# Kernel tuning notes

Measured on AMD Instinct MI355X. Metric: run time of the kernel, lower is better.

## Reference

```python
import jax, jax.numpy as jnp
import numpy as np

H, DQK, DV, DM, POS = 8, 64, 64, 768, 64

def _rel_basis(l, n):
    # Enformer central-mask relative position basis: [l, l, n]
    pos = jnp.arange(l)
    distance = pos[None, :] - pos[:, None]              # [l, l] int
    half = n // 2
    pow_rate = jnp.exp(jnp.log(jnp.asarray((l + 1) / 2.0, jnp.float32)) / half)
    center_widths = pow_rate ** jnp.arange(1, half + 1, dtype=jnp.float32)  # [half]
    unsigned = (jnp.abs(distance)[:, :, None].astype(jnp.float32) <= center_widths)
    signed = jnp.sign(distance)[:, :, None] * unsigned
    return jnp.concatenate([unsigned.astype(jnp.float32), signed.astype(jnp.float32)], axis=-1)

def setup_inputs() -> dict:
    key = jax.random.key(0)
    ks = jax.random.split(key, 9)
    b, l = 2, 1024
    x = jax.random.normal(ks[0], (b, l, DM), jnp.float32)
    # torch Linear weights: [out, in]
    Wq = jax.random.normal(ks[1], (H * DQK, DM), jnp.float32) * (1.0 / np.sqrt(DM))
    Wk = jax.random.normal(ks[2], (H * DQK, DM), jnp.float32) * (1.0 / np.sqrt(DM))
    Wv = jax.random.normal(ks[3], (H * DV, DM), jnp.float32) * (1.0 / np.sqrt(DM))
    Wo = jax.random.normal(ks[4], (DM, H * DV), jnp.float32) * (1.0 / np.sqrt(H * DV))
    bo = jnp.zeros((DM,), jnp.float32)
    u_bias = jax.random.normal(ks[5], (H, DQK), jnp.float32) * np.sqrt(2.0 / DQK)
    v_bias = jax.random.normal(ks[6], (H, DQK), jnp.float32) * np.sqrt(2.0 / DQK)
    w_pos = jax.random.normal(ks[7], (H, DQK, POS), jnp.float32) * np.sqrt(2.0 / POS)
    return {"x": x, "Wq": Wq, "Wk": Wk, "Wv": Wv, "Wo": Wo, "bo": bo,
            "u_bias": u_bias, "v_bias": v_bias, "w_pos": w_pos}

def reference(x, Wq, Wk, Wv, Wo, bo, u_bias, v_bias, w_pos):
    b, l, _ = x.shape
    q = (x @ Wq.T).reshape(b, l, H, DQK)
    k = (x @ Wk.T).reshape(b, l, H, DQK)
    v = (x @ Wv.T).reshape(b, l, H, DV)
    basis = _rel_basis(l, POS)                           # [l, l, n]
    scale = 1.0 / np.sqrt(DQK)
    # qr_term: einsum('bihd,hdn,ijn->bhij') factored to avoid [b,h,l,l,d]
    qw = jnp.einsum('bihd,hdn->bhin', q, w_pos)          # [b,h,l,n]
    qr = jnp.einsum('bhin,ijn->bhij', qw, basis)
    uk = jnp.einsum('hd,bjhd->bhj', u_bias, k)[:, :, None, :]
    vw = jnp.einsum('hd,hdn->hn', v_bias, w_pos)
    vr = jnp.einsum('hn,ijn->hij', vw, basis)[None]      # [1,h,l,l]
    bias = (qr + uk + vr) * scale
    scores = jnp.einsum('bihd,bjhd->bhij', q, k) * scale + bias
    attn = jax.nn.softmax(scores, axis=-1)
    out = jnp.einsum('bhij,bjhd->bihd', attn, v).reshape(b, l, H * DV)
    return out @ Wo.T + bo
```

## Files before the change

### kernel.cpp

```cpp
#include <hip/hip_runtime.h>

#define LSEQ 1024
#define NB   2
#define NH   8
#define DD   64
#define DMOD 768

using bf16x8 = __attribute__((ext_vector_type(8))) short;
using f32x4  = __attribute__((ext_vector_type(4))) float;

__device__ inline unsigned short f2bf(float f) {
    union { float f; unsigned u; } v; v.f = f;
    unsigned r = v.u + 0x7FFFu + ((v.u >> 16) & 1u);
    return (unsigned short)(r >> 16);
}

__global__ __launch_bounds__(256) void pack_setup(
    const float4* __restrict__ x,  const float4* __restrict__ wq,
    const float4* __restrict__ wk, const float4* __restrict__ wv,
    const float4* __restrict__ wo,
    const float* __restrict__ u_bias, const float* __restrict__ v_bias,
    const float* __restrict__ w_pos,
    ushort4* __restrict__ xb, ushort4* __restrict__ wqb, ushort4* __restrict__ wkb,
    ushort4* __restrict__ wvb, ushort4* __restrict__ wob,
    float* __restrict__ wsfx, unsigned char* __restrict__ cls_g)
{
    int tid = threadIdx.x;
    if (blockIdx.x >= 3072) {
        int sb = blockIdx.x - 3072;
        if (sb == 0) {
            __shared__ float w_s[32];
            __shared__ int cmin_s[1024];
            if (tid < 32) {
                float pr = expf(logf(512.5f) / 32.0f);
                w_s[tid] = powf(pr, (float)(tid + 1));
            }
            __syncthreads();
            for (int d = tid; d < 1024; d += 256) {
                float fd = (float)d;
                int cm = 32;
                for (int c = 31; c >= 0; --c) if (fd <= w_s[c]) cm = c;
                cmin_s[d] = cm;
            }
            __syncthreads();
            for (int d2 = tid; d2 < 2048; d2 += 256) {
                int dd = d2 - 1023;
                int ad = dd < 0 ? -dd : dd; if (ad > 1023) ad = 1023;
                int t = (dd < 0) ? 0 : ((dd == 0) ? 1 : 2);
                cls_g[d2] = (unsigned char)(t * 33 + cmin_s[ad]);
            }
        } else {
            int h = sb - 1;
            __shared__ float vred[4][64];
            __shared__ float ured[4][64];
            __shared__ float wd[64];
            int n = tid & 63, g = tid >> 6;
            float vs = 0.f, us = 0.f;
#pragma unroll
            for (int k = 0; k < 16; ++k) {
                int d = g * 16 + k;
                float wp = w_pos[(h * 64 + d) * 64 + n];
                vs += v_bias[h * 64 + d] * wp;
                us += u_bias[h * 64 + d] * wp;
            }
            vred[g][n] = vs; ured[g][n] = us;
            __syncthreads();
            if (tid < 64) {
                float v4 = vred[0][tid] + vred[1][tid] + vred[2][tid] + vred[3][tid];
                float u4 = ured[0][tid] + ured[1][tid] + ured[2][tid] + ured[3][tid];
                wd[tid] = v4 - u4;
            }
            __syncthreads();
            if (tid < 64) {
                int nn = tid & 31, cb = tid & 32;
                float s = 0.f;
                for (int c = 31; c >= nn; --c) s += wd[cb + c];
                wsfx[h * 64 + tid] = s * 0.125f;
            }
        }
        return;
    }
    int i = blockIdx.x * 256 + tid;
    const float4* src; ushort4* dst; int off;
    if (i < 393216)      { src = x;  dst = xb;  off = i; }
    else if (i < 491520) { src = wq; dst = wqb; off = i - 393216; }
    else if (i < 589824) { src = wk; dst = wkb; off = i - 491520; }
    else if (i < 688128) { src = wv; dst = wvb; off = i - 589824; }
    else                 { src = wo; dst = wob; off = i - 688128; }
    float4 v = src[off];
    ushort4 o;
    o.x = f2bf(v.x); o.y = f2bf(v.y); o.z = f2bf(v.z); o.w = f2bf(v.w);
    dst[off] = o;
}

__global__ __launch_bounds__(256) void gemm_qkv(
    const unsigned short* __restrict__ X, const unsigned short* __restrict__ W,
    const float* __restrict__ ub,
    unsigned short* __restrict__ Qb, unsigned short* __restrict__ Kb,
    unsigned short* __restrict__ Vtb)
{
    __shared__ __align__(16) unsigned short Xs[2][64][72];
    __shared__ __align__(16) unsigned short Wsm[2][64][72];
    __shared__ __align__(16) unsigned short Ct[64][72];

    int tid = threadIdx.x;
    int w = tid >> 6, lane = tid & 63, l15 = lane & 15, q = lane >> 4;
    int M0 = blockIdx.y * 64, N0 = blockIdx.x * 64;
    int rs = tid >> 3, seg = tid & 3 ? (tid & 7) : (tid & 7);
    seg = tid & 7;

    const unsigned short* xp = X + (size_t)(M0 + rs) * 768 + seg * 8;
    const unsigned short* wp = W + (size_t)(N0 + rs) * 768 + seg * 8;

    uint4 xa = *(const uint4*)(xp);
    uint4 xb = *(const uint4*)(xp + (size_t)32 * 768);
    uint4 wa = *(const uint4*)(wp);
    uint4 wb = *(const uint4*)(wp + (size_t)32 * 768);

    f32x4 acc[4] = {};
    int cur = 0;
    for (int k0 = 0; k0 < 768; k0 += 64) {
        *(uint4*)&Xs[cur][rs][seg * 8]       = xa;
        *(uint4*)&Xs[cur][rs + 32][seg * 8]  = xb;
        *(uint4*)&Wsm[cur][rs][seg * 8]      = wa;
        *(uint4*)&Wsm[cur][rs + 32][seg * 8] = wb;
        __syncthreads();
        if (k0 + 64 < 768) {
            xa = *(const uint4*)(xp + k0 + 64);
            xb = *(const uint4*)(xp + (size_t)32 * 768 + k0 + 64);
            wa = *(const uint4*)(wp + k0 + 64);
            wb = *(const uint4*)(wp + (size_t)32 * 768 + k0 + 64);
        }
        bf16x8 a0 = *(bf16x8*)&Xs[cur][w * 16 + l15][q * 8];
        bf16x8 a1 = *(bf16x8*)&Xs[cur][w * 16 + l15][32 + q * 8];
#pragma unroll
        for (int ct = 0; ct < 4; ++ct) {
            bf16x8 b0 = *(bf16x8*)&Wsm[cur][ct * 16 + l15][q * 8];
            bf16x8 b1 = *(bf16x8*)&Wsm[cur][ct * 16 + l15][32 + q * 8];
            acc[ct] = __builtin_amdgcn_mfma_f32_16x16x32_bf16(a0, b0, acc[ct], 0, 0, 0);
            acc[ct] = __builtin_amdgcn_mfma_f32_16x16x32_bf16(a1, b1, acc[ct], 0, 0, 0);
        }
        cur ^= 1;
    }

    if (N0 < 1024) {
        int isQ = (N0 < 512);
#pragma unroll
        for (int ct = 0; ct < 4; ++ct) {
            float u0 = isQ ? ub[N0 + ct * 16 + l15] : 0.f;
            float sc = isQ ? 0.125f : 1.0f;
#pragma unroll
            for (int r = 0; r < 4; ++r)
                Ct[w * 16 + q * 4 + r][ct * 16 + l15] = f2bf((acc[ct][r] + u0) * sc);
        }
        __syncthreads();
        int Nh = isQ ? N0 : (N0 - 512);
        unsigned short* out = isQ ? Qb : Kb;
        size_t base = ((size_t)((M0 >> 10) * 8 + (Nh >> 6)) * 1024 + (M0 & 1023)) * 64;
#pragma unroll
        for (int it = 0; it < 2; ++it) {
            int idx = tid + it * 256;
            int row = idx >> 3, sg = idx & 7;
            *(uint4*)(out + base + (size_t)row * 64 + sg * 8) = *(uint4*)&Ct[row][sg * 8];
        }
    } else {
#pragma unroll
        for (int ct = 0; ct < 4; ++ct) {
            ushort4 pk;
            pk.x = f2bf(acc[ct][0]); pk.y = f2bf(acc[ct][1]);
            pk.z = f2bf(acc[ct][2]); pk.w = f2bf(acc[ct][3]);
            *(ushort4*)&Ct[ct * 16 + l15][w * 16 + q * 4] = pk;
        }
        __syncthreads();
        size_t base = ((size_t)((M0 >> 10) * 8 + ((N0 - 1024) >> 6))) * 65536;
        int j0 = M0 & 1023;
#pragma unroll
        for (int it = 0; it < 2; ++it) {
            int idx = tid + it * 256;
            int d = idx >> 3, sg = idx & 7;
            *(uint4*)(Vtb + base + (size_t)d * 1024 + j0 + sg * 8) = *(uint4*)&Ct[d][sg * 8];
        }
    }
}

__global__ __launch_bounds__(256) void gemm_o(
    const unsigned short* __restrict__ X, const unsigned short* __restrict__ W,
    const float* __restrict__ bias, float* __restrict__ out)
{
    __shared__ __align__(16) unsigned short Xs[2][64][72];
    __shared__ __align__(16) unsigned short Wsm[2][64][72];
    __shared__ __align__(16) float Ctf[64][72];

    int tid = threadIdx.x;
    int w = tid >> 6, lane = tid & 63, l15 = lane & 15, q = lane >> 4;
    int M0 = blockIdx.y * 64, N0 = blockIdx.x * 64;
    int rs = tid >> 3, seg = tid & 7;

    const unsigned short* xp = X + (size_t)(M0 + rs) * 512 + seg * 8;
    const unsigned short* wp = W + (size_t)(N0 + rs) * 512 + seg * 8;

    uint4 xa = *(const uint4*)(xp);
    uint4 xb = *(const uint4*)(xp + (size_t)32 * 512);
    uint4 wa = *(const uint4*)(wp);
    uint4 wb = *(const uint4*)(wp + (size_t)32 * 512);

    f32x4 acc[4] = {};
    int cur = 0;
    for (int k0 = 0; k0 < 512; k0 += 64) {
        *(uint4*)&Xs[cur][rs][seg * 8]       = xa;
        *(uint4*)&Xs[cur][rs + 32][seg * 8]  = xb;
        *(uint4*)&Wsm[cur][rs][seg * 8]      = wa;
        *(uint4*)&Wsm[cur][rs + 32][seg * 8] = wb;
        __syncthreads();
        if (k0 + 64 < 512) {
            xa = *(const uint4*)(xp + k0 + 64);
            xb = *(const uint4*)(xp + (size_t)32 * 512 + k0 + 64);
            wa = *(const uint4*)(wp + k0 + 64);
            wb = *(const uint4*)(wp + (size_t)32 * 512 + k0 + 64);
        }
        bf16x8 a0 = *(bf16x8*)&Xs[cur][w * 16 + l15][q * 8];
        bf16x8 a1 = *(bf16x8*)&Xs[cur][w * 16 + l15][32 + q * 8];
#pragma unroll
        for (int ct = 0; ct < 4; ++ct) {
            bf16x8 b0 = *(bf16x8*)&Wsm[cur][ct * 16 + l15][q * 8];
            bf16x8 b1 = *(bf16x8*)&Wsm[cur][ct * 16 + l15][32 + q * 8];
            acc[ct] = __builtin_amdgcn_mfma_f32_16x16x32_bf16(a0, b0, acc[ct], 0, 0, 0);
            acc[ct] = __builtin_amdgcn_mfma_f32_16x16x32_bf16(a1, b1, acc[ct], 0, 0, 0);
        }
        cur ^= 1;
    }
#pragma unroll
    for (int ct = 0; ct < 4; ++ct) {
        float bv = bias[N0 + ct * 16 + l15];
#pragma unroll
        for (int r = 0; r < 4; ++r)
            Ctf[w * 16 + q * 4 + r][ct * 16 + l15] = acc[ct][r] + bv;
    }
    __syncthreads();
#pragma unroll
    for (int it = 0; it < 4; ++it) {
        int idx = tid + it * 256;
        int row = idx >> 4, sg = idx & 15;
        *(float4*)(out + (size_t)(M0 + row) * 768 + N0 + sg * 4) = *(float4*)&Ctf[row][sg * 4];
    }
}

__global__ __launch_bounds__(256, 4) void attn_mfma(
    const unsigned short* __restrict__ Qbf,
    const unsigned short* __restrict__ Kbf,
    const unsigned short* __restrict__ Vt,
    const float* __restrict__ w_pos,
    const float* __restrict__ wsfx,
    const unsigned char* __restrict__ cls_g,
    unsigned short* __restrict__ ao)
{
    __shared__ float biasT[16 * 99];
    __shared__ unsigned char cls[2048];
    __shared__ unsigned short Pl[4][16][76];
    union Ovl {
        struct { unsigned short wptS[64][68]; float qwL[16][68]; } pre;
        struct { float Obuf[4][64][17]; float lbuf[4][16]; } post;
    };
    __shared__ Ovl ovl;

    int tid = threadIdx.x;
    int b = blockIdx.z, h = blockIdx.y, bh = b * 8 + h;
    int i0 = blockIdx.x * 16;
    int w = tid >> 6, lane = tid & 63, l15 = lane & 15, q = lane >> 4;

    for (int idx = tid; idx < 512; idx += 256)
        ((unsigned int*)cls)[idx] = ((const unsigned int*)cls_g)[idx];
    {
        const float4* wsrc = (const float4*)(w_pos + h * 4096);
#pragma unroll
        for (int it = 0; it < 4; ++it) {
            int f = tid + it * 256;
            float4 wv = wsrc[f];
            int d = f >> 4, n4 = (f & 15) * 4;
            ovl.pre.wptS[n4 + 0][d] = f2bf(wv.x);
            ovl.pre.wptS[n4 + 1][d] = f2bf(wv.y);
            ovl.pre.wptS[n4 + 2][d] = f2bf(wv.z);
            ovl.pre.wptS[n4 + 3][d] = f2bf(wv.w);
        }
    }

    int ig = i0 + l15;
    const unsigned short* qrow = Qbf + ((size_t)bh * 1024 + ig) * 64;
    bf16x8 qf0 = *(const bf16x8*)(qrow + q * 8);
    bf16x8 qf1 = *(const bf16x8*)(qrow + 32 + q * 8);
    __syncthreads();

    {
        bf16x8 b0 = *(bf16x8*)&ovl.pre.wptS[w * 16 + l15][q * 8];
        bf16x8 b1 = *(bf16x8*)&ovl.pre.wptS[w * 16 + l15][32 + q * 8];
        f32x4 a = {};
        a = __builtin_amdgcn_mfma_f32_16x16x32_bf16(qf0, b0, a, 0, 0, 0);
        a = __builtin_amdgcn_mfma_f32_16x16x32_bf16(qf1, b1, a, 0, 0, 0);
#pragma unroll
        for (int r = 0; r < 4; ++r)
            ovl.pre.qwL[q * 4 + r][w * 16 + l15] = a[r];
    }
    __syncthreads();

    const float* wsh = wsfx + h * 64;
#pragma unroll
    for (int it = 0; it < 4; ++it) {
        int idx = tid + it * 256;
        int il = idx >> 6, n = idx & 63, nn = n & 31, cb = n & 32;
        float run = 0.f, s = 0.f;
#pragma unroll
        for (int c = 31; c >= 0; --c) {
            run += ovl.pre.qwL[il][cb + c];
            if (c == nn) s = run;
        }
        ovl.pre.qwL[il][n] = s + wsh[n];
    }
    __syncthreads();

    for (int idx = tid; idx < 528; idx += 256) {
        int il = idx / 33, c = idx - il * 33;
        float up = 0.f, sp = 0.f;
        if (c < 32) {
            up = ovl.pre.qwL[il][c];
            sp = ovl.pre.qwL[il][32 + c];
        }
        float* bt = biasT + il * 99;
        bt[c]      = up - sp;
        bt[33 + c] = up;
        bt[66 + c] = up + sp;
    }
    __syncthreads();

    const unsigned short* Kbase = Kbf + (size_t)bh * 65536;
    const unsigned short* Vbase = Vt  + (size_t)bh * 65536;
    const float* btrow = biasT + l15 * 99;
    int clsoff = 1023 - ig;

    f32x4 Oacc[4] = {};
    float lsum = 0.f;

    for (int jt = 0; jt < 4; ++jt) {
        int jb = w * 256 + jt * 64;
        f32x4 st[4];
        __builtin_amdgcn_s_setprio(1);
#pragma unroll
        for (int ct = 0; ct < 4; ++ct) {
            const unsigned short* krow = Kbase + (size_t)(jb + ct * 16 + l15) * 64;
            bf16x8 ka0 = *(const bf16x8*)(krow + q * 8);
            bf16x8 ka1 = *(const bf16x8*)(krow + 32 + q * 8);
            f32x4 a = {};
            a = __builtin_amdgcn_mfma_f32_16x16x32_bf16(ka0, qf0, a, 0, 0, 0);
            a = __builtin_amdgcn_mfma_f32_16x16x32_bf16(ka1, qf1, a, 0, 0, 0);
            st[ct] = a;
        }
        __builtin_amdgcn_s_setprio(0);
#pragma unroll
        for (int ct = 0; ct < 4; ++ct) {
            int d2b = jb + ct * 16 + q * 4 + clsoff;
            float pv[4];
#pragma unroll
            for (int r = 0; r < 4; ++r) {
                float s = st[ct][r] + btrow[cls[d2b + r]];
                float p = __expf(s);
                lsum += p;
                pv[r] = p;
            }
            ushort4 pk;
            pk.x = f2bf(pv[0]); pk.y = f2bf(pv[1]);
            pk.z = f2bf(pv[2]); pk.w = f2bf(pv[3]);
            *(ushort4*)&Pl[w][l15][ct * 16 + q * 4] = pk;
        }
        __builtin_amdgcn_s_setprio(1);
#pragma unroll
        for (int ks = 0; ks < 2; ++ks) {
            bf16x8 pb = *(const bf16x8*)&Pl[w][l15][ks * 32 + q * 8];
#pragma unroll
            for (int dt = 0; dt < 4; ++dt) {
                bf16x8 va = *(const bf16x8*)(Vbase + (size_t)(dt * 16 + l15) * 1024
                                             + jb + ks * 32 + q * 8);
                Oacc[dt] = __builtin_amdgcn_mfma_f32_16x16x32_bf16(va, pb, Oacc[dt], 0, 0, 0);
            }
        }
        __builtin_amdgcn_s_setprio(0);
    }

    lsum += __shfl_xor(lsum, 16);
    lsum += __shfl_xor(lsum, 32);

    __syncthreads();
#pragma unroll
    for (int dt = 0; dt < 4; ++dt)
#pragma unroll
        for (int r = 0; r < 4; ++r)
            ovl.post.Obuf[w][dt * 16 + q * 4 + r][l15] = Oacc[dt][r];
    if (lane < 16) ovl.post.lbuf[w][l15] = lsum;
    __syncthreads();

    for (int t2 = tid; t2 < 1024; t2 += 256) {
        int il = t2 >> 6, d = t2 & 63;
        float o = ovl.post.Obuf[0][d][il] + ovl.post.Obuf[1][d][il]
                + ovl.post.Obuf[2][d][il] + ovl.post.Obuf[3][d][il];
        float l = ovl.post.lbuf[0][il] + ovl.post.lbuf[1][il]
                + ovl.post.lbuf[2][il] + ovl.post.lbuf[3][il];
        ao[((size_t)(b * 1024 + i0 + il)) * 512 + h * 64 + d] = f2bf(o / l);
    }
}

extern "C" void kernel_launch(void* const* d_in, const int* in_sizes, int n_in,
                              void* d_out, int out_size, void* d_ws, size_t ws_size,
                              hipStream_t stream)
{
    const float* x      = (const float*)d_in[0];
    const float* Wq     = (const float*)d_in[1];
    const float* Wk     = (const float*)d_in[2];
    const float* Wv     = (const float*)d_in[3];
    const float* Wo     = (const float*)d_in[4];
    const float* bo     = (const float*)d_in[5];
    const float* u_bias = (const float*)d_in[6];
    const float* v_bias = (const float*)d_in[7];
    const float* w_pos  = (const float*)d_in[8];
    float* out = (float*)d_out;

    char* ws = (char*)d_ws;
    unsigned short* Xbf  = (unsigned short*)ws;            ws += 3145728;
    unsigned short* Wqkv = (unsigned short*)ws;            ws += 2359296;
    unsigned short* Wob  = (unsigned short*)ws;            ws += 786432;
    unsigned short* Qbf  = (unsigned short*)ws;            ws += 2097152;
    unsigned short* Kbf  = (unsigned short*)ws;            ws += 2097152;
    unsigned short* Vtb  = (unsigned short*)ws;            ws += 2097152;
    unsigned short* aob  = (unsigned short*)ws;            ws += 2097152;
    float*          wsfx = (float*)ws;                     ws += 2048;
    unsigned char*  clsg = (unsigned char*)ws;             ws += 2048;

    pack_setup<<<3081, 256, 0, stream>>>(
        (const float4*)x, (const float4*)Wq, (const float4*)Wk,
        (const float4*)Wv, (const float4*)Wo,
        u_bias, v_bias, w_pos,
        (ushort4*)Xbf,
        (ushort4*)Wqkv, (ushort4*)Wqkv + 98304, (ushort4*)Wqkv + 196608,
        (ushort4*)Wob,
        wsfx, clsg);

    gemm_qkv<<<dim3(24, 32), 256, 0, stream>>>(Xbf, Wqkv, u_bias, Qbf, Kbf, Vtb);

    attn_mfma<<<dim3(64, 8, 2), 256, 0, stream>>>(
        Qbf, Kbf, Vtb, w_pos, wsfx, clsg, aob);

    gemm_o<<<dim3(12, 32), 256, 0, stream>>>(aob, Wob, bo, out);
}
```

Baseline: 133.1 us.

## Split qw/bias-table prologue out of attention into a separate kernel

Moves the per-row q·w_pos projection, suffix-sum and bias-table construction from the attention kernel's prologue into a new qw_bias kernel that writes a per-row 99-entry bias table to global workspace. The attention kernel then only copies its 16 rows of that table into shared memory, dropping three barriers and the shared union. The suffix sum now uses warp shuffles instead of a serial 32-step loop. In exchange this adds a kernel launch and about 6.5 MB of extra global writes and reads.

Result: slower. 140.1 us (+5.3%).

```diff
diff --git a/kernel.cpp b/kernel.cpp
--- a/kernel.cpp
+++ b/kernel.cpp
@@ -106,8 +106,7 @@
     int tid = threadIdx.x;
     int w = tid >> 6, lane = tid & 63, l15 = lane & 15, q = lane >> 4;
     int M0 = blockIdx.y * 64, N0 = blockIdx.x * 64;
-    int rs = tid >> 3, seg = tid & 3 ? (tid & 7) : (tid & 7);
-    seg = tid & 7;
+    int rs = tid >> 3, seg = tid & 7;
 
     const unsigned short* xp = X + (size_t)(M0 + rs) * 768 + seg * 8;
     const unsigned short* wp = W + (size_t)(N0 + rs) * 768 + seg * 8;
@@ -245,23 +244,86 @@
     }
 }
 
+__global__ __launch_bounds__(256) void qw_bias(
+    const unsigned short* __restrict__ Qbf,
+    const float* __restrict__ w_pos,
+    const float* __restrict__ wsfx,
+    float* __restrict__ bias_g)
+{
+    __shared__ unsigned short wptS[64][68];
+    __shared__ float qwL[64][68];
+
+    int tid = threadIdx.x;
+    int bh = blockIdx.y, h = bh & 7;
+    int i0 = blockIdx.x * 64;
+    int w = tid >> 6, lane = tid & 63, l15 = lane & 15, q = lane >> 4;
+
+    const float4* wsrc = (const float4*)(w_pos + h * 4096);
+#pragma unroll
+    for (int it = 0; it < 4; ++it) {
+        int f = tid + it * 256;
+        float4 wv4 = wsrc[f];
+        int d = f >> 4, n4 = (f & 15) * 4;
+        wptS[n4 + 0][d] = f2bf(wv4.x);
+        wptS[n4 + 1][d] = f2bf(wv4.y);
+        wptS[n4 + 2][d] = f2bf(wv4.z);
+        wptS[n4 + 3][d] = f2bf(wv4.w);
+    }
+    int ig = i0 + w * 16 + l15;
+    const unsigned short* qrow = Qbf + ((size_t)bh * 1024 + ig) * 64;
+    bf16x8 qf0 = *(const bf16x8*)(qrow + q * 8);
+    bf16x8 qf1 = *(const bf16x8*)(qrow + 32 + q * 8);
+    __syncthreads();
+
+#pragma unroll
+    for (int ct = 0; ct < 4; ++ct) {
+        bf16x8 b0 = *(bf16x8*)&wptS[ct * 16 + l15][q * 8];
+        bf16x8 b1 = *(bf16x8*)&wptS[ct * 16 + l15][32 + q * 8];
+        f32x4 a = {};
+        a = __builtin_amdgcn_mfma_f32_16x16x32_bf16(qf0, b0, a, 0, 0, 0);
+        a = __builtin_amdgcn_mfma_f32_16x16x32_bf16(qf1, b1, a, 0, 0, 0);
+#pragma unroll
+        for (int r = 0; r < 4; ++r)
+            qwL[w * 16 + q * 4 + r][ct * 16 + l15] = a[r];
+    }
+    __syncthreads();
+
+    float wv = wsfx[h * 64 + lane];
+    int c = lane & 31;
+    for (int rr = 0; rr < 16; ++rr) {
+        int i = w * 16 + rr;
+        float s = qwL[i][lane];
+#pragma unroll
+        for (int off = 1; off < 32; off <<= 1) {
+            float t = __shfl_down(s, off, 32);
+            if (c + off < 32) s += t;
+        }
+        s += wv;
+        float o = __shfl_xor(s, 32);
+        float* bt = bias_g + ((size_t)bh * 1024 + i0 + i) * 99;
+        if (lane < 32) {
+            bt[c]      = s - o;
+            bt[33 + c] = s;
+            bt[66 + c] = s + o;
+        } else if (lane == 32) {
+            bt[32] = 0.f; bt[65] = 0.f; bt[98] = 0.f;
+        }
+    }
+}
+
 __global__ __launch_bounds__(256, 4) void attn_mfma(
     const unsigned short* __restrict__ Qbf,
     const unsigned short* __restrict__ Kbf,
     const unsigned short* __restrict__ Vt,
-    const float* __restrict__ w_pos,
-    const float* __restrict__ wsfx,
+    const float* __restrict__ bias_g,
     const unsigned char* __restrict__ cls_g,
     unsigned short* __restrict__ ao)
 {
     __shared__ float biasT[16 * 99];
     __shared__ unsigned char cls[2048];
     __shared__ unsigned short Pl[4][16][76];
-    union Ovl {
-        struct { unsigned short wptS[64][68]; float qwL[16][68]; } pre;
-        struct { float Obuf[4][64][17]; float lbuf[4][16]; } post;
-    };
-    __shared__ Ovl ovl;
+    __shared__ float Obuf[4][64][17];
+    __shared__ float lbuf[4][16];
 
     int tid = threadIdx.x;
     int b = blockIdx.z, h = blockIdx.y, bh = b * 8 + h;
@@ -271,64 +333,15 @@
     for (int idx = tid; idx < 512; idx += 256)
         ((unsigned int*)cls)[idx] = ((const unsigned int*)cls_g)[idx];
     {
-        const float4* wsrc = (const float4*)(w_pos + h * 4096);
-#pragma unroll
-        for (int it = 0; it < 4; ++it) {
-            int f = tid + it * 256;
-            float4 wv = wsrc[f];
-            int d = f >> 4, n4 = (f & 15) * 4;
-            ovl.pre.wptS[n4 + 0][d] = f2bf(wv.x);
-            ovl.pre.wptS[n4 + 1][d] = f2bf(wv.y);
-            ovl.pre.wptS[n4 + 2][d] = f2bf(wv.z);
-            ovl.pre.wptS[n4 + 3][d] = f2bf(wv.w);
-        }
+        const float* src = bias_g + ((size_t)bh * 1024 + i0) * 99;
+        for (int idx = tid; idx < 1584; idx += 256)
+            biasT[idx] = src[idx];
     }
 
     int ig = i0 + l15;
     const unsigned short* qrow = Qbf + ((size_t)bh * 1024 + ig) * 64;
     bf16x8 qf0 = *(const bf16x8*)(qrow + q * 8);
     bf16x8 qf1 = *(const bf16x8*)(qrow + 32 + q * 8);
-    __syncthreads();
-
-    {
-        bf16x8 b0 = *(bf16x8*)&ovl.pre.wptS[w * 16 + l15][q * 8];
-        bf16x8 b1 = *(bf16x8*)&ovl.pre.wptS[w * 16 + l15][32 + q * 8];
-        f32x4 a = {};
-        a = __builtin_amdgcn_mfma_f32_16x16x32_bf16(qf0, b0, a, 0, 0, 0);
-        a = __builtin_amdgcn_mfma_f32_16x16x32_bf16(qf1, b1, a, 0, 0, 0);
-#pragma unroll
-        for (int r = 0; r < 4; ++r)
-            ovl.pre.qwL[q * 4 + r][w * 16 + l15] = a[r];
-    }
-    __syncthreads();
-
-    const float* wsh = wsfx + h * 64;
-#pragma unroll
-    for (int it = 0; it < 4; ++it) {
-        int idx = tid + it * 256;
-        int il = idx >> 6, n = idx & 63, nn = n & 31, cb = n & 32;
-        float run = 0.f, s = 0.f;
-#pragma unroll
-        for (int c = 31; c >= 0; --c) {
-            run += ovl.pre.qwL[il][cb + c];
-            if (c == nn) s = run;
-        }
-        ovl.pre.qwL[il][n] = s + wsh[n];
-    }
-    __syncthreads();
-
-    for (int idx = tid; idx < 528; idx += 256) {
-        int il = idx / 33, c = idx - il * 33;
-        float up = 0.f, sp = 0.f;
-        if (c < 32) {
-            up = ovl.pre.qwL[il][c];
-            sp = ovl.pre.qwL[il][32 + c];
-        }
-        float* bt = biasT + il * 99;
-        bt[c]      = up - sp;
-        bt[33 + c] = up;
-        bt[66 + c] = up + sp;
-    }
     __syncthreads();
 
     const unsigned short* Kbase = Kbf + (size_t)bh * 65536;
@@ -387,21 +400,20 @@
     lsum += __shfl_xor(lsum, 16);
     lsum += __shfl_xor(lsum, 32);
 
-    __syncthreads();
 #pragma unroll
     for (int dt = 0; dt < 4; ++dt)
 #pragma unroll
         for (int r = 0; r < 4; ++r)
-            ovl.post.Obuf[w][dt * 16 + q * 4 + r][l15] = Oacc[dt][r];
-    if (lane < 16) ovl.post.lbuf[w][l15] = lsum;
+            Obuf[w][dt * 16 + q * 4 + r][l15] = Oacc[dt][r];
+    if (lane < 16) lbuf[w][l15] = lsum;
     __syncthreads();
 
     for (int t2 = tid; t2 < 1024; t2 += 256) {
         int il = t2 >> 6, d = t2 & 63;
-        float o = ovl.post.Obuf[0][d][il] + ovl.post.Obuf[1][d][il]
-                + ovl.post.Obuf[2][d][il] + ovl.post.Obuf[3][d][il];
-        float l = ovl.post.lbuf[0][il] + ovl.post.lbuf[1][il]
-                + ovl.post.lbuf[2][il] + ovl.post.lbuf[3][il];
+        float o = Obuf[0][d][il] + Obuf[1][d][il]
+                + Obuf[2][d][il] + Obuf[3][d][il];
+        float l = lbuf[0][il] + lbuf[1][il]
+                + lbuf[2][il] + lbuf[3][il];
         ao[((size_t)(b * 1024 + i0 + il)) * 512 + h * 64 + d] = f2bf(o / l);
     }
 }
@@ -431,6 +443,7 @@
     unsigned short* aob  = (unsigned short*)ws;            ws += 2097152;
     float*          wsfx = (float*)ws;                     ws += 2048;
     unsigned char*  clsg = (unsigned char*)ws;             ws += 2048;
+    float*          biasg = (float*)ws;                    ws += 6488064;
 
     pack_setup<<<3081, 256, 0, stream>>>(
         (const float4*)x, (const float4*)Wq, (const float4*)Wk,
@@ -443,8 +456,10 @@
 
     gemm_qkv<<<dim3(24, 32), 256, 0, stream>>>(Xbf, Wqkv, u_bias, Qbf, Kbf, Vtb);
 
+    qw_bias<<<dim3(16, 16), 256, 0, stream>>>(Qbf, w_pos, wsfx, biasg);
+
     attn_mfma<<<dim3(64, 8, 2), 256, 0, stream>>>(
-        Qbf, Kbf, Vtb, w_pos, wsfx, clsg, aob);
+        Qbf, Kbf, Vtb, biasg, clsg, aob);
 
     gemm_o<<<dim3(12, 32), 256, 0, stream>>>(aob, Wob, bo, out);
 }
```

## Fuse fp32-to-bf16 packing into QKV and output GEMM loaders, drop pack kernel

Applied to the files above, without the earlier changes.

Removes the separate pack_setup kernel. The GEMMs now read fp32 x and the weights directly and convert them to bf16 while staging tiles into shared memory. The small setup work (the position-class table and the per-head bias suffix sums) moves into an extra row of blocks in the QKV GEMM grid, reusing its shared memory. This saves one kernel launch and the round trip of writing and re-reading bf16 copies, but each GEMM block now loads twice as many bytes per tile, and the weights are converted again by every M-tile.

After: 134.3 us. About the same (+0.9%).

```diff
diff --git a/kernel.cpp b/kernel.cpp
--- a/kernel.cpp
+++ b/kernel.cpp
@@ -15,22 +15,37 @@
     return (unsigned short)(r >> 16);
 }
 
-__global__ __launch_bounds__(256) void pack_setup(
-    const float4* __restrict__ x,  const float4* __restrict__ wq,
-    const float4* __restrict__ wk, const float4* __restrict__ wv,
-    const float4* __restrict__ wo,
-    const float* __restrict__ u_bias, const float* __restrict__ v_bias,
+__device__ inline uint4 pk8(float4 a, float4 b) {
+    uint4 o;
+    o.x = (unsigned)f2bf(a.x) | ((unsigned)f2bf(a.y) << 16);
+    o.y = (unsigned)f2bf(a.z) | ((unsigned)f2bf(a.w) << 16);
+    o.z = (unsigned)f2bf(b.x) | ((unsigned)f2bf(b.y) << 16);
+    o.w = (unsigned)f2bf(b.z) | ((unsigned)f2bf(b.w) << 16);
+    return o;
+}
+
+__global__ __launch_bounds__(256) void gemm_qkv(
+    const float* __restrict__ X,
+    const float* __restrict__ Wqp, const float* __restrict__ Wkp,
+    const float* __restrict__ Wvp,
+    const float* __restrict__ ub,
+    const float* __restrict__ v_bias,
     const float* __restrict__ w_pos,
-    ushort4* __restrict__ xb, ushort4* __restrict__ wqb, ushort4* __restrict__ wkb,
-    ushort4* __restrict__ wvb, ushort4* __restrict__ wob,
+    unsigned short* __restrict__ Qb, unsigned short* __restrict__ Kb,
+    unsigned short* __restrict__ Vtb,
     float* __restrict__ wsfx, unsigned char* __restrict__ cls_g)
 {
+    __shared__ __align__(16) unsigned short Xs[2][64][72];
+    __shared__ __align__(16) unsigned short Wsm[2][64][72];
+    __shared__ __align__(16) unsigned short Ct[64][72];
+
     int tid = threadIdx.x;
-    if (blockIdx.x >= 3072) {
-        int sb = blockIdx.x - 3072;
+
+    if (blockIdx.y == 32) {
+        int sb = blockIdx.x;
         if (sb == 0) {
-            __shared__ float w_s[32];
-            __shared__ int cmin_s[1024];
+            float* w_s   = (float*)&Ct[0][0];
+            int*   cmin_s = (int*)&Ct[1][0];
             if (tid < 32) {
                 float pr = expf(logf(512.5f) / 32.0f);
                 w_s[tid] = powf(pr, (float)(tid + 1));
@@ -49,11 +64,11 @@
                 int t = (dd < 0) ? 0 : ((dd == 0) ? 1 : 2);
                 cls_g[d2] = (unsigned char)(t * 33 + cmin_s[ad]);
             }
-        } else {
+        } else if (sb <= 8) {
             int h = sb - 1;
-            __shared__ float vred[4][64];
-            __shared__ float ured[4][64];
-            __shared__ float wd[64];
+            float (*vred)[64] = (float(*)[64])&Ct[0][0];
+            float (*ured)[64] = (float(*)[64])&Ct[8][0];
+            float* wd = (float*)&Ct[16][0];
             int n = tid & 63, g = tid >> 6;
             float vs = 0.f, us = 0.f;
 #pragma unroll
@@ -61,7 +76,7 @@
                 int d = g * 16 + k;
                 float wp = w_pos[(h * 64 + d) * 64 + n];
                 vs += v_bias[h * 64 + d] * wp;
-                us += u_bias[h * 64 + d] * wp;
+                us += ub[h * 64 + d] * wp;
             }
             vred[g][n] = vs; ured[g][n] = us;
             __syncthreads();
@@ -80,57 +95,38 @@
         }
         return;
     }
-    int i = blockIdx.x * 256 + tid;
-    const float4* src; ushort4* dst; int off;
-    if (i < 393216)      { src = x;  dst = xb;  off = i; }
-    else if (i < 491520) { src = wq; dst = wqb; off = i - 393216; }
-    else if (i < 589824) { src = wk; dst = wkb; off = i - 491520; }
-    else if (i < 688128) { src = wv; dst = wvb; off = i - 589824; }
-    else                 { src = wo; dst = wob; off = i - 688128; }
-    float4 v = src[off];
-    ushort4 o;
-    o.x = f2bf(v.x); o.y = f2bf(v.y); o.z = f2bf(v.z); o.w = f2bf(v.w);
-    dst[off] = o;
-}
-
-__global__ __launch_bounds__(256) void gemm_qkv(
-    const unsigned short* __restrict__ X, const unsigned short* __restrict__ W,
-    const float* __restrict__ ub,
-    unsigned short* __restrict__ Qb, unsigned short* __restrict__ Kb,
-    unsigned short* __restrict__ Vtb)
-{
-    __shared__ __align__(16) unsigned short Xs[2][64][72];
-    __shared__ __align__(16) unsigned short Wsm[2][64][72];
-    __shared__ __align__(16) unsigned short Ct[64][72];
-
-    int tid = threadIdx.x;
+
     int w = tid >> 6, lane = tid & 63, l15 = lane & 15, q = lane >> 4;
     int M0 = blockIdx.y * 64, N0 = blockIdx.x * 64;
-    int rs = tid >> 3, seg = tid & 3 ? (tid & 7) : (tid & 7);
-    seg = tid & 7;
-
-    const unsigned short* xp = X + (size_t)(M0 + rs) * 768 + seg * 8;
-    const unsigned short* wp = W + (size_t)(N0 + rs) * 768 + seg * 8;
-
-    uint4 xa = *(const uint4*)(xp);
-    uint4 xb = *(const uint4*)(xp + (size_t)32 * 768);
-    uint4 wa = *(const uint4*)(wp);
-    uint4 wb = *(const uint4*)(wp + (size_t)32 * 768);
+    int rs = tid >> 3, seg = tid & 7;
+
+    const float* Wsrc; int Nr;
+    if (N0 < 512)       { Wsrc = Wqp; Nr = N0; }
+    else if (N0 < 1024) { Wsrc = Wkp; Nr = N0 - 512; }
+    else                { Wsrc = Wvp; Nr = N0 - 1024; }
+
+    const float* xp = X    + (size_t)(M0 + rs) * 768 + seg * 8;
+    const float* wp = Wsrc + (size_t)(Nr + rs) * 768 + seg * 8;
+
+    float4 xa0, xa1, xb0, xb1, wa0, wa1, wb0, wb1;
+#define LOADQ(K) do { \
+    xa0 = *(const float4*)(xp + (K));               xa1 = *(const float4*)(xp + (K) + 4); \
+    xb0 = *(const float4*)(xp + 32 * 768 + (K));    xb1 = *(const float4*)(xp + 32 * 768 + (K) + 4); \
+    wa0 = *(const float4*)(wp + (K));               wa1 = *(const float4*)(wp + (K) + 4); \
+    wb0 = *(const float4*)(wp + 32 * 768 + (K));    wb1 = *(const float4*)(wp + 32 * 768 + (K) + 4); \
+} while (0)
+
+    LOADQ(0);
 
     f32x4 acc[4] = {};
     int cur = 0;
     for (int k0 = 0; k0 < 768; k0 += 64) {
-        *(uint4*)&Xs[cur][rs][seg * 8]       = xa;
-        *(uint4*)&Xs[cur][rs + 32][seg * 8]  = xb;
-        *(uint4*)&Wsm[cur][rs][seg * 8]      = wa;
-        *(uint4*)&Wsm[cur][rs + 32][seg * 8] = wb;
+        *(uint4*)&Xs[cur][rs][seg * 8]       = pk8(xa0, xa1);
+        *(uint4*)&Xs[cur][rs + 32][seg * 8]  = pk8(xb0, xb1);
+        *(uint4*)&Wsm[cur][rs][seg * 8]      = pk8(wa0, wa1);
+        *(uint4*)&Wsm[cur][rs + 32][seg * 8] = pk8(wb0, wb1);
         __syncthreads();
-        if (k0 + 64 < 768) {
-            xa = *(const uint4*)(xp + k0 + 64);
-            xb = *(const uint4*)(xp + (size_t)32 * 768 + k0 + 64);
-            wa = *(const uint4*)(wp + k0 + 64);
-            wb = *(const uint4*)(wp + (size_t)32 * 768 + k0 + 64);
-        }
+        if (k0 + 64 < 768) LOADQ(k0 + 64);
         bf16x8 a0 = *(bf16x8*)&Xs[cur][w * 16 + l15][q * 8];
         bf16x8 a1 = *(bf16x8*)&Xs[cur][w * 16 + l15][32 + q * 8];
 #pragma unroll
@@ -142,6 +138,7 @@
         }
         cur ^= 1;
     }
+#undef LOADQ
 
     if (N0 < 1024) {
         int isQ = (N0 < 512);
@@ -184,7 +181,8 @@
 }
 
 __global__ __launch_bounds__(256) void gemm_o(
-    const unsigned short* __restrict__ X, const unsigned short* __restrict__ W,
+    const unsigned short* __restrict__ X,
+    const float* __restrict__ W,
     const float* __restrict__ bias, float* __restrict__ out)
 {
     __shared__ __align__(16) unsigned short Xs[2][64][72];
@@ -197,27 +195,28 @@
     int rs = tid >> 3, seg = tid & 7;
 
     const unsigned short* xp = X + (size_t)(M0 + rs) * 512 + seg * 8;
-    const unsigned short* wp = W + (size_t)(N0 + rs) * 512 + seg * 8;
-
-    uint4 xa = *(const uint4*)(xp);
-    uint4 xb = *(const uint4*)(xp + (size_t)32 * 512);
-    uint4 wa = *(const uint4*)(wp);
-    uint4 wb = *(const uint4*)(wp + (size_t)32 * 512);
+    const float*          wp = W + (size_t)(N0 + rs) * 512 + seg * 8;
+
+    uint4 xa, xb;
+    float4 wa0, wa1, wb0, wb1;
+#define LOADO(K) do { \
+    xa  = *(const uint4*)(xp + (K)); \
+    xb  = *(const uint4*)(xp + 32 * 512 + (K)); \
+    wa0 = *(const float4*)(wp + (K));            wa1 = *(const float4*)(wp + (K) + 4); \
+    wb0 = *(const float4*)(wp + 32 * 512 + (K)); wb1 = *(const float4*)(wp + 32 * 512 + (K) + 4); \
+} while (0)
+
+    LOADO(0);
 
     f32x4 acc[4] = {};
     int cur = 0;
     for (int k0 = 0; k0 < 512; k0 += 64) {
         *(uint4*)&Xs[cur][rs][seg * 8]       = xa;
         *(uint4*)&Xs[cur][rs + 32][seg * 8]  = xb;
-        *(uint4*)&Wsm[cur][rs][seg * 8]      = wa;
-        *(uint4*)&Wsm[cur][rs + 32][seg * 8] = wb;
+        *(uint4*)&Wsm[cur][rs][seg * 8]      = pk8(wa0, wa1);
+        *(uint4*)&Wsm[cur][rs + 32][seg * 8] = pk8(wb0, wb1);
         __syncthreads();
-        if (k0 + 64 < 512) {
-            xa = *(const uint4*)(xp + k0 + 64);
-            xb = *(const uint4*)(xp + (size_t)32 * 512 + k0 + 64);
-            wa = *(const uint4*)(wp + k0 + 64);
-            wb = *(const uint4*)(wp + (size_t)32 * 512 + k0 + 64);
-        }
+        if (k0 + 64 < 512) LOADO(k0 + 64);
         bf16x8 a0 = *(bf16x8*)&Xs[cur][w * 16 + l15][q * 8];
         bf16x8 a1 = *(bf16x8*)&Xs[cur][w * 16 + l15][32 + q * 8];
 #pragma unroll
@@ -229,6 +228,7 @@
         }
         cur ^= 1;
     }
+#undef LOADO
 #pragma unroll
     for (int ct = 0; ct < 4; ++ct) {
         float bv = bias[N0 + ct * 16 + l15];
@@ -422,9 +422,6 @@
     float* out = (float*)d_out;
 
     char* ws = (char*)d_ws;
-    unsigned short* Xbf  = (unsigned short*)ws;            ws += 3145728;
-    unsigned short* Wqkv = (unsigned short*)ws;            ws += 2359296;
-    unsigned short* Wob  = (unsigned short*)ws;            ws += 786432;
     unsigned short* Qbf  = (unsigned short*)ws;            ws += 2097152;
     unsigned short* Kbf  = (unsigned short*)ws;            ws += 2097152;
     unsigned short* Vtb  = (unsigned short*)ws;            ws += 2097152;
@@ -432,19 +429,11 @@
     float*          wsfx = (float*)ws;                     ws += 2048;
     unsigned char*  clsg = (unsigned char*)ws;             ws += 2048;
 
-    pack_setup<<<3081, 256, 0, stream>>>(
-        (const float4*)x, (const float4*)Wq, (const float4*)Wk,
-        (const float4*)Wv, (const float4*)Wo,
-        u_bias, v_bias, w_pos,
-        (ushort4*)Xbf,
-        (ushort4*)Wqkv, (ushort4*)Wqkv + 98304, (ushort4*)Wqkv + 196608,
-        (ushort4*)Wob,
-        wsfx, clsg);
-
-    gemm_qkv<<<dim3(24, 32), 256, 0, stream>>>(Xbf, Wqkv, u_bias, Qbf, Kbf, Vtb);
+    gemm_qkv<<<dim3(24, 33), 256, 0, stream>>>(
+        x, Wq, Wk, Wv, u_bias, v_bias, w_pos, Qbf, Kbf, Vtb, wsfx, clsg);
 
     attn_mfma<<<dim3(64, 8, 2), 256, 0, stream>>>(
         Qbf, Kbf, Vtb, w_pos, wsfx, clsg, aob);
 
-    gemm_o<<<dim3(12, 32), 256, 0, stream>>>(aob, Wob, bo, out);
-}
+    gemm_o<<<dim3(12, 32), 256, 0, stream>>>(aob, Wo, bo, out);
+}
```
